# Kernel optimization log

Measured on AMD Instinct MI355X. Metric: run time of the kernel, lower is better.

The kernel has to match this reference:

```python
import jax, jax.numpy as jnp
import numpy as np

B, V = 128, 128256

def setup_inputs() -> dict:
    key = jax.random.key(0)
    k1, k2, k3, k4, k5 = jax.random.split(key, 5)
    logits = jax.random.normal(k1, (B, V), dtype=jnp.float32) * 2.0
    temperatures = jax.random.uniform(k2, (B,), dtype=jnp.float32) * 0.9 + 0.3  # [0.3, 1.2)
    top_ks = jax.random.randint(k3, (B,), 1, 65, dtype=jnp.int32)               # in [1, 64]
    top_ps = jax.random.uniform(k4, (B,), dtype=jnp.float32) * 0.85 + 0.1       # [0.1, 0.95)
    u = jax.random.uniform(k5, (B,), dtype=jnp.float32)                          # multinomial draw
    return {"logits": logits, "temperatures": temperatures, "top_ks": top_ks,
            "top_ps": top_ps, "u": u}

def reference(logits, temperatures, top_ks, top_ps, u):
    # logits /= temperatures ; probs = softmax(logits)
    probs = jax.nn.softmax(logits / temperatures[:, None], axis=-1)  # [B, V]
    # descending sort (argsort then gather so the permutation is explicit)
    idx = jnp.argsort(-probs, axis=-1)                               # [B, V] int
    probs_sort = jnp.take_along_axis(probs, idx, axis=-1)            # [B, V]
    probs_sum = jnp.cumsum(probs_sort, axis=-1)
    # top-p filter: zero where cumulative mass BEFORE this token exceeds top_p
    # top-k filter: zero beyond rank top_k
    ranks = jnp.arange(probs.shape[-1], dtype=jnp.int32)[None, :]
    mask = (probs_sum - probs_sort > top_ps[:, None]) | (ranks >= top_ks[:, None])
    probs_sort = jnp.where(mask, 0.0, probs_sort)
    # torch code divides by row max (multinomial renormalizes anyway)
    probs_sort = probs_sort / jnp.max(probs_sort, axis=-1, keepdims=True)
    # multinomial(num_samples=1) via inverse-CDF with one uniform per row
    cdf = jnp.cumsum(probs_sort, axis=-1)                            # [B, V]
    r = u[:, None] * cdf[:, -1:]
    sampled_rank = jnp.sum((cdf < r).astype(jnp.int32), axis=-1)     # [B]
    sampled_rank = jnp.clip(sampled_rank, 0, probs.shape[-1] - 1)
    batch_next_token_ids = jnp.take_along_axis(idx, sampled_rank[:, None], axis=-1)[:, 0]
    success = jnp.ones((probs.shape[0],), dtype=jnp.bool_)
    return batch_next_token_ids.astype(jnp.int32), success, probs_sort
```

## Files before the change

### kernel.cpp

```cpp
#include <hip/hip_runtime.h>
#include <math.h>

namespace {
constexpr int kB = 128;
constexpr int kV = 128256;
constexpr int kSplits = 16;
constexpr int kSplit = kV / kSplits;
constexpr int kSplit4 = kSplit / 4;
constexpr int kT1 = 256;
constexpr int kE = 8;
constexpr int kCap = 256;
constexpr int kTop = 64;

using f4v = __attribute__((ext_vector_type(4))) float;

__device__ __forceinline__ unsigned fkey(float y) {
  unsigned u = __float_as_uint(y);
  return ((int)u < 0) ? ~u : (u | 0x80000000u);
}
__device__ __forceinline__ float keyinv(unsigned k) {
  unsigned u = (k & 0x80000000u) ? (k & 0x7fffffffu) : ~k;
  return __uint_as_float(u);
}

__global__ __launch_bounds__(kT1) void k_select(
    const float* __restrict__ logits, const float* __restrict__ temps,
    float* __restrict__ out,
    float* __restrict__ wm, float* __restrict__ wS,
    unsigned long long* __restrict__ wpk) {
  const int sp = blockIdx.x, row = blockIdx.y, tid = threadIdx.x;
  const int lane = tid & 63, wid = tid >> 6;
  __shared__ float wred[4];
  __shared__ float ssum[4];
  __shared__ int cnt2[2][4];
  __shared__ unsigned long long cand[kCap];
  __shared__ int scnt;

  if (tid == 0) scnt = 0;
  const float t = temps[row];
  const float invt = 1.0f / t;
  const size_t rowbase = (size_t)row * kV + (size_t)sp * kSplit;
  const float4* in4 = (const float4*)(logits + rowbase);
  f4v* out4 = (f4v*)(out + 2 * kB + rowbase);
  const float nI = -INFINITY;

  float4 r[kE];
  float m = nI;
#pragma unroll
  for (int e = 0; e < kE; ++e) {
    int f = tid + e * kT1;
    float4 l;
    if (f < kSplit4) l = in4[f];
    else l = make_float4(nI, nI, nI, nI);
    r[e] = l;
    m = fmaxf(m, fmaxf(fmaxf(l.x, l.y), fmaxf(l.z, l.w)));
  }
  for (int o = 32; o; o >>= 1) m = fmaxf(m, __shfl_xor(m, o));
  if (lane == 0) wred[wid] = m;
  __syncthreads();
  const float M = fmaxf(fmaxf(wred[0], wred[1]), fmaxf(wred[2], wred[3]));
  const float My = M / t;
  const float negMy = -My;

  {
    const f4v z4 = {0.f, 0.f, 0.f, 0.f};
#pragma unroll
    for (int e = 0; e < kE; ++e) {
      int f = tid + e * kT1;
      if (f < kSplit4) __builtin_nontemporal_store(z4, out4 + f);
    }
  }

  float s = 0.f;
#pragma unroll
  for (int e = 0; e < kE; ++e) {
    s += __expf(fmaf(r[e].x, invt, negMy));
    s += __expf(fmaf(r[e].y, invt, negMy));
    s += __expf(fmaf(r[e].z, invt, negMy));
    s += __expf(fmaf(r[e].w, invt, negMy));
  }
  for (int o = 32; o; o >>= 1) s += __shfl_xor(s, o);
  if (lane == 0) ssum[wid] = s;
  __syncthreads();
  const float Ssp = ssum[0] + ssum[1] + ssum[2] + ssum[3];

  unsigned lo = 0x00800000u;
  unsigned hi = fkey(M) + 1;
  for (int it = 0; it < 32 && hi - lo > 1; ++it) {
    unsigned mid = lo + ((hi - lo) >> 1);
    if (it == 0) {
      unsigned p0 = fkey(M - 3.0f);
      if (p0 > lo && p0 < hi) mid = p0;
    } else if (it == 1) {
      unsigned p1 = fkey(M - 4.5f);
      if (p1 > lo && p1 < hi) mid = p1;
    }
    const float mf = keyinv(mid);
    int cw = 0;
#pragma unroll
    for (int e = 0; e < kE; ++e) {
      cw += (int)__popcll(__ballot(r[e].x >= mf));
      cw += (int)__popcll(__ballot(r[e].y >= mf));
      cw += (int)__popcll(__ballot(r[e].z >= mf));
      cw += (int)__popcll(__ballot(r[e].w >= mf));
    }
    if (lane == 0) cnt2[it & 1][wid] = cw;
    __syncthreads();
    const int c = cnt2[it & 1][0] + cnt2[it & 1][1] +
                  cnt2[it & 1][2] + cnt2[it & 1][3];
    if (c >= kTop) { lo = mid; if (c <= kCap) break; }
    else hi = mid;
  }
  const float Tf = keyinv(lo);

#pragma unroll
  for (int e = 0; e < kE; ++e) {
    int f = tid + e * kT1;
    const float vals[4] = {r[e].x, r[e].y, r[e].z, r[e].w};
#pragma unroll
    for (int j = 0; j < 4; ++j) {
      const float lv = vals[j];
      if (lv >= Tf) {
        int pos = atomicAdd(&scnt, 1);
        if (pos < kCap)
          cand[pos] = ((unsigned long long)fkey(lv) << 32) |
                      (unsigned)~(unsigned)(sp * kSplit + f * 4 + j);
      }
    }
  }
  __syncthreads();
  const int nc = scnt < kCap ? scnt : kCap;
  unsigned long long v = (tid < nc) ? cand[tid] : 0ULL;

  for (int k2 = 2; k2 <= kCap; k2 <<= 1) {
    for (int j = k2 >> 1; j; j >>= 1) {
      unsigned long long o;
      if (j < 64) {
        o = __shfl_xor(v, j);
      } else {
        __syncthreads();
        cand[tid] = v;
        __syncthreads();
        o = cand[tid ^ j];
      }
      const bool keep_max = (((tid & k2) == 0) == ((tid & j) == 0));
      v = keep_max ? (o > v ? o : v) : (o < v ? o : v);
    }
  }

  if (tid < kTop)
    wpk[((size_t)row * kSplits + sp) * kTop + tid] = v;
  if (tid == 0) {
    wm[row * kSplits + sp] = My;
    wS[row * kSplits + sp] = Ssp;
  }
}

__global__ __launch_bounds__(kT1) void k_sample(
    const float* __restrict__ temps,
    const int* __restrict__ top_ks, const float* __restrict__ top_ps,
    const float* __restrict__ uin,
    const float* __restrict__ wm, const float* __restrict__ wS,
    const unsigned long long* __restrict__ wpk, float* __restrict__ out) {
  const int row = blockIdx.x, tid = threadIdx.x;
  constexpr int kN = kSplits * kTop;
  __shared__ unsigned long long pk[kN];
  __shared__ float mArr[kSplits], sArr[kSplits];
  __shared__ float tv[kTop];
  __shared__ int ti[kTop];
  __shared__ float sv[kTop];
  __shared__ float MS[2];

  if (tid < kSplits) {
    mArr[tid] = wm[row * kSplits + tid];
    sArr[tid] = wS[row * kSplits + tid];
  }
  for (int i = tid; i < kN; i += kT1)
    pk[i] = wpk[(size_t)row * kN + i];
  __syncthreads();
  if (tid == 0) {
    float M = -INFINITY;
    for (int s2 = 0; s2 < kSplits; ++s2) M = fmaxf(M, mArr[s2]);
    float S = 0.f;
    for (int s2 = 0; s2 < kSplits; ++s2) S += expf(mArr[s2] - M) * sArr[s2];
    MS[0] = M; MS[1] = S;
  }

  for (int r = 0; r < 4; ++r) {
    const int pairs = 8 >> r;
    __syncthreads();
    for (int w = tid; w < pairs * 64; w += kT1) {
      int q = w >> 6, i = w & 63;
      int a = q * (128 << r), b = a + (64 << r);
      unsigned long long x = pk[a + i], y = pk[b + 63 - i];
      pk[a + i] = x > y ? x : y;
    }
    for (int j = 32; j; j >>= 1) {
      __syncthreads();
      for (int w = tid; w < pairs * 32; w += kT1) {
        int q = w >> 5, z = w & 31;
        int a = q * (128 << r);
        int i = ((z & ~(j - 1)) << 1) | (z & (j - 1));
        unsigned long long x = pk[a + i], y = pk[a + i + j];
        if (x < y) { pk[a + i] = y; pk[a + i + j] = x; }
      }
    }
  }
  __syncthreads();

  if (tid < kTop) {
    unsigned long long p2 = pk[tid];
    tv[tid] = keyinv((unsigned)(p2 >> 32)) / temps[row];
    ti[tid] = (int)(~(unsigned)(p2 & 0xffffffffu));
  }
  __syncthreads();

  if (tid == 0) {
    const float M = MS[0], S = MS[1];
    const float tp = top_ps[row];
    const int kk = top_ks[row];
    const float uu = uin[row];
    float cum = 0.f;
    float qa[kTop];
#pragma unroll
    for (int r = 0; r < kTop; ++r) {
      float pr = expf(tv[r] - M) / S;
      cum += pr;
      float cb = cum - pr;
      qa[r] = ((cb > tp) || (r >= kk)) ? 0.f : pr;
    }
    const float q0 = qa[0];
    float tot = 0.f;
    float cdfa[kTop];
#pragma unroll
    for (int r = 0; r < kTop; ++r) {
      float sr = qa[r] / q0;
      sv[r] = sr;
      tot += sr;
      cdfa[r] = tot;
    }
    const float rth = uu * tot;
    int cnt = 0;
#pragma unroll
    for (int r = 0; r < kTop; ++r) cnt += (cdfa[r] < rth) ? 1 : 0;
    if (cnt > kTop - 1) cnt = kTop - 1;
    out[row] = (float)ti[cnt];
    out[kB + row] = 1.0f;
  }
  __syncthreads();
  if (tid < kTop) out[2 * kB + (size_t)row * kV + tid] = sv[tid];
}
}

extern "C" void kernel_launch(void* const* d_in, const int* in_sizes, int n_in,
                              void* d_out, int out_size, void* d_ws, size_t ws_size,
                              hipStream_t stream) {
  const float* logits = (const float*)d_in[0];
  const float* temps  = (const float*)d_in[1];
  const int*   top_ks = (const int*)d_in[2];
  const float* top_ps = (const float*)d_in[3];
  const float* uin    = (const float*)d_in[4];
  float* out = (float*)d_out;

  float* wm = (float*)d_ws;
  float* wS = wm + kB * kSplits;
  unsigned long long* wpk =
      (unsigned long long*)(wS + kB * kSplits + kB * kSplits);

  k_select<<<dim3(kSplits, kB), kT1, 0, stream>>>(logits, temps, out, wm, wS, wpk);
  k_sample<<<kB, kT1, 0, stream>>>(temps, top_ks, top_ps, uin, wm, wS, wpk, out);
}
```

Measured before the change: 51.00 us.

## Rewrite sampling kernel as single-wavefront register merge with shuffles

The sampling kernel drops from 256 threads to one 64-lane wavefront. The 16 per-split sorted top-64 lists are now merged in registers by repeated bitonic merge steps using shuffles, which removes the shared-memory merge and its many block barriers. The serial single-thread top-p/top-k and CDF loops become wavefront-cooperative, using shuffles plus a ballot/popcount for the sampled rank. The merge is now sequential across 16 splits with 6 shuffle steps each, so it trades parallel width for fewer syncs. The second kernel is small relative to the main selection kernel.

```diff
diff --git a/kernel.cpp b/kernel.cpp
--- a/kernel.cpp
+++ b/kernel.cpp
@@ -156,99 +156,68 @@
   }
 }
 
-__global__ __launch_bounds__(kT1) void k_sample(
+__global__ __launch_bounds__(64) void k_sample(
     const float* __restrict__ temps,
     const int* __restrict__ top_ks, const float* __restrict__ top_ps,
     const float* __restrict__ uin,
     const float* __restrict__ wm, const float* __restrict__ wS,
     const unsigned long long* __restrict__ wpk, float* __restrict__ out) {
-  const int row = blockIdx.x, tid = threadIdx.x;
-  constexpr int kN = kSplits * kTop;
-  __shared__ unsigned long long pk[kN];
-  __shared__ float mArr[kSplits], sArr[kSplits];
-  __shared__ float tv[kTop];
-  __shared__ int ti[kTop];
-  __shared__ float sv[kTop];
-  __shared__ float MS[2];
-
-  if (tid < kSplits) {
-    mArr[tid] = wm[row * kSplits + tid];
-    sArr[tid] = wS[row * kSplits + tid];
-  }
-  for (int i = tid; i < kN; i += kT1)
-    pk[i] = wpk[(size_t)row * kN + i];
-  __syncthreads();
-  if (tid == 0) {
-    float M = -INFINITY;
-    for (int s2 = 0; s2 < kSplits; ++s2) M = fmaxf(M, mArr[s2]);
-    float S = 0.f;
-    for (int s2 = 0; s2 < kSplits; ++s2) S += expf(mArr[s2] - M) * sArr[s2];
-    MS[0] = M; MS[1] = S;
-  }
-
-  for (int r = 0; r < 4; ++r) {
-    const int pairs = 8 >> r;
-    __syncthreads();
-    for (int w = tid; w < pairs * 64; w += kT1) {
-      int q = w >> 6, i = w & 63;
-      int a = q * (128 << r), b = a + (64 << r);
-      unsigned long long x = pk[a + i], y = pk[b + 63 - i];
-      pk[a + i] = x > y ? x : y;
-    }
+  const int row = blockIdx.x;
+  const int lane = threadIdx.x;
+
+  float M = -INFINITY;
+  for (int s2 = 0; s2 < kSplits; ++s2) M = fmaxf(M, wm[row * kSplits + s2]);
+  float S = 0.f;
+  for (int s2 = 0; s2 < kSplits; ++s2)
+    S += expf(wm[row * kSplits + s2] - M) * wS[row * kSplits + s2];
+
+  const unsigned long long* base = wpk + (size_t)row * (kSplits * kTop);
+  unsigned long long v = base[lane];
+  for (int s2 = 1; s2 < kSplits; ++s2) {
+    unsigned long long b = base[s2 * kTop + (kTop - 1 - lane)];
+    v = v > b ? v : b;
+#pragma unroll
     for (int j = 32; j; j >>= 1) {
-      __syncthreads();
-      for (int w = tid; w < pairs * 32; w += kT1) {
-        int q = w >> 5, z = w & 31;
-        int a = q * (128 << r);
-        int i = ((z & ~(j - 1)) << 1) | (z & (j - 1));
-        unsigned long long x = pk[a + i], y = pk[a + i + j];
-        if (x < y) { pk[a + i] = y; pk[a + i + j] = x; }
-      }
-    }
-  }
-  __syncthreads();
-
-  if (tid < kTop) {
-    unsigned long long p2 = pk[tid];
-    tv[tid] = keyinv((unsigned)(p2 >> 32)) / temps[row];
-    ti[tid] = (int)(~(unsigned)(p2 & 0xffffffffu));
-  }
-  __syncthreads();
-
-  if (tid == 0) {
-    const float M = MS[0], S = MS[1];
-    const float tp = top_ps[row];
-    const int kk = top_ks[row];
-    const float uu = uin[row];
-    float cum = 0.f;
-    float qa[kTop];
-#pragma unroll
-    for (int r = 0; r < kTop; ++r) {
-      float pr = expf(tv[r] - M) / S;
-      cum += pr;
-      float cb = cum - pr;
-      qa[r] = ((cb > tp) || (r >= kk)) ? 0.f : pr;
-    }
-    const float q0 = qa[0];
-    float tot = 0.f;
-    float cdfa[kTop];
-#pragma unroll
-    for (int r = 0; r < kTop; ++r) {
-      float sr = qa[r] / q0;
-      sv[r] = sr;
-      tot += sr;
-      cdfa[r] = tot;
-    }
-    const float rth = uu * tot;
-    int cnt = 0;
-#pragma unroll
-    for (int r = 0; r < kTop; ++r) cnt += (cdfa[r] < rth) ? 1 : 0;
-    if (cnt > kTop - 1) cnt = kTop - 1;
-    out[row] = (float)ti[cnt];
+      unsigned long long o = __shfl_xor(v, j);
+      v = ((lane & j) == 0) ? (v > o ? v : o) : (v < o ? v : o);
+    }
+  }
+  const float tvl = keyinv((unsigned)(v >> 32)) / temps[row];
+  const int til = (int)(~(unsigned)(v & 0xffffffffu));
+
+  const float tp = top_ps[row];
+  const int kk = top_ks[row];
+  const float uu = uin[row];
+
+  float cum = 0.f, q0 = 0.f;
+  float qa_keep = 0.f;
+  for (int r2 = 0; r2 < kTop; ++r2) {
+    const float tvr = __shfl(tvl, r2);
+    const float pr = expf(tvr - M) / S;
+    cum += pr;
+    const float cb = cum - pr;
+    const float q = ((cb > tp) || (r2 >= kk)) ? 0.f : pr;
+    if (r2 == 0) q0 = q;
+    if (lane == r2) qa_keep = q;
+  }
+  float tot = 0.f;
+  float sv_keep = 0.f, cdf_keep = 0.f;
+  for (int r2 = 0; r2 < kTop; ++r2) {
+    const float qr = __shfl(qa_keep, r2);
+    const float sr = qr / q0;
+    tot += sr;
+    if (lane == r2) { sv_keep = sr; cdf_keep = tot; }
+  }
+  const float rth = uu * tot;
+  int cnt = (int)__popcll(__ballot(cdf_keep < rth));
+  if (cnt > kTop - 1) cnt = kTop - 1;
+  const int sampled = __shfl(til, cnt);
+
+  if (lane == 0) {
+    out[row] = (float)sampled;
     out[kB + row] = 1.0f;
   }
-  __syncthreads();
-  if (tid < kTop) out[2 * kB + (size_t)row * kV + tid] = sv[tid];
+  out[2 * kB + (size_t)row * kV + lane] = sv_keep;
 }
 }
 
@@ -268,5 +237,5 @@
       (unsigned long long*)(wS + kB * kSplits + kB * kSplits);
 
   k_select<<<dim3(kSplits, kB), kT1, 0, stream>>>(logits, temps, out, wm, wS, wpk);
-  k_sample<<<kB, kT1, 0, stream>>>(temps, top_ks, top_ps, uin, wm, wS, wpk, out);
-}
+  k_sample<<<kB, 64, 0, stream>>>(temps, top_ks, top_ps, uin, wm, wS, wpk, out);
+}
```

Result: slower. 55.32 us (+8.5%).
